# Performance work log

Hardware: AMD Instinct MI355X
Metric: run time of the kernel (lower is better)

Reference implementation:

```python
import jax, jax.numpy as jnp
import numpy as np

P1 = np.uint32(2654435761)
P2 = np.uint32(805459861)

LEVELS = 16
N_MIN = 16
GROWTH = 1.5
TABLE_SIZE = 524288
FEAT_DIM = 2


def _make_seeds_u32(levels):
    cA = np.uint64(15485907386658061715)
    cB = np.uint64(11400714819323198485)
    ls = np.arange(levels, dtype=np.uint64)
    u = (cA ^ (ls * cB))  # uint64 wraparound
    return (u & np.uint64(0xFFFFFFFF)).astype(np.uint32)


def setup_inputs() -> dict:
    key = jax.random.key(0)
    k1, k2, k3 = jax.random.split(key, 3)
    B = 8
    H = 256
    tile = 1024
    x0 = jax.random.uniform(k1, (B,), dtype=jnp.float32) * (tile - H)
    y0 = jax.random.uniform(k2, (B,), dtype=jnp.float32) * (tile - H)
    tables = jax.random.uniform(k3, (TABLE_SIZE, FEAT_DIM), dtype=jnp.float32,
                                minval=-0.01, maxval=0.01)
    seeds = jnp.asarray(_make_seeds_u32(LEVELS))
    level_N = jnp.asarray(
        [int(round(N_MIN * GROWTH ** l)) for l in range(LEVELS)], dtype=jnp.float32)
    return {"x0": x0, "y0": y0, "tables": tables, "seeds": seeds,
            "level_N": level_N, "memorized_crop_size": H,
            "complete_tile_size": tile}


def _hash2d(ix, iy, seed_u, T):
    # Instant-NGP style spatial hash, uint32 wraparound, per-level seed.
    h = (ix.astype(jnp.uint32) * P1) ^ (iy.astype(jnp.uint32) * P2) ^ seed_u
    return (h % jnp.uint32(T)).astype(jnp.int32)


def reference(x0, y0, tables, seeds, level_N, memorized_crop_size, complete_tile_size):
    B = x0.shape[0]
    H = W = int(memorized_crop_size)
    L = seeds.shape[0]
    T, F = tables.shape
    N = H * W

    xs = jnp.arange(H, dtype=jnp.float32)
    yy, xx = jnp.meshgrid(xs, xs, indexing='ij')          # [H, W]
    pxf = (xx[None] + x0[:, None, None]).reshape(B, N)     # [B, N]
    pyf = (yy[None] + y0[:, None, None]).reshape(B, N)

    scales = level_N / jnp.float32(complete_tile_size)     # [L]
    xyn_x = pxf[:, None, :] * scales[None, :, None]        # [B, L, N]
    xyn_y = pyf[:, None, :] * scales[None, :, None]

    ix0 = jnp.floor(xyn_x).astype(jnp.int32)
    iy0 = jnp.floor(xyn_y).astype(jnp.int32)
    ix1 = ix0 + 1
    iy1 = iy0 + 1
    fx = (xyn_x - ix0)[..., None]                          # [B, L, N, 1]
    fy = (xyn_y - iy0)[..., None]

    s = seeds[None, :, None]                               # [1, L, 1] uint32
    f00 = tables[_hash2d(ix0, iy0, s, T)]                  # [B, L, N, F]
    f10 = tables[_hash2d(ix1, iy0, s, T)]
    f01 = tables[_hash2d(ix0, iy1, s, T)]
    f11 = tables[_hash2d(ix1, iy1, s, T)]

    enc = ((1.0 - fx) * (1.0 - fy) * f00 + fx * (1.0 - fy) * f10
           + (1.0 - fx) * fy * f01 + fx * fy * f11)        # [B, L, N, F]

    enc = jnp.transpose(enc, (0, 2, 1, 3)).reshape(B, H, W, L * F)
    return jnp.transpose(enc, (0, 3, 1, 2))                # [B, L*F, H, W]
```

## Files before the change

kernel.cpp:

```cpp
#include <hip/hip_runtime.h>
#include <stdint.h>

#define HASH_T 524288u
#define HASH_MASK (HASH_T - 1u)
#define PRIME1 2654435761u
#define PRIME2 805459861u


#define HASHES(l, h00, h10, h01, h11, FX, FY)                          \
    float FX, FY; uint32_t h00, h10, h01, h11;                         \
    {                                                                  \
        const float s_ = level_N[l] * inv_tile;                        \
        const float xn_ = px * s_, yn_ = py * s_;                      \
        const int ix_ = (int)xn_, iy_ = (int)yn_;     \
        FX = xn_ - (float)ix_; FY = yn_ - (float)iy_;                  \
        const uint32_t hx0_ = (uint32_t)ix_ * PRIME1, hx1_ = hx0_ + PRIME1; \
        const uint32_t hy0_ = (uint32_t)iy_ * PRIME2, hy1_ = hy0_ + PRIME2; \
        const uint32_t sd_ = seeds[l];                                 \
        h00 = (hx0_ ^ hy0_ ^ sd_) & HASH_MASK;                         \
        h10 = (hx1_ ^ hy0_ ^ sd_) & HASH_MASK;                         \
        h01 = (hx0_ ^ hy1_ ^ sd_) & HASH_MASK;                         \
        h11 = (hx1_ ^ hy1_ ^ sd_) & HASH_MASK;                         \
    }

#define LOADS(h00, h10, h01, h11, f00, f10, f01, f11)                  \
    const float2 f00 = tab2[h00], f10 = tab2[h10],                     \
                 f01 = tab2[h01], f11 = tab2[h11];

#define STOREL(l, FX, FY, f00, f10, f01, f11)                          \
    {                                                                  \
        const float gx_ = 1.0f - FX, gy_ = 1.0f - FY;                  \
        const float w00_ = gx_ * gy_, w10_ = FX * gy_;                 \
        const float w01_ = gx_ * FY,  w11_ = FX * FY;                  \
        const float e0_ = w00_ * f00.x + w10_ * f10.x + w01_ * f01.x + w11_ * f11.x; \
        const float e1_ = w00_ * f00.y + w10_ * f10.y + w01_ * f01.y + w11_ * f11.y; \
        __builtin_nontemporal_store(e0_, outp + (size_t)(2 * (l)) * 65536u);     \
        __builtin_nontemporal_store(e1_, outp + (size_t)(2 * (l) + 1) * 65536u); \
    }

#define PAIR(la, lb)                                                   \
    {                                                                  \
        HASHES(la, a00, a10, a01, a11, fxa, fya)                       \
        HASHES(lb, b00, b10, b01, b11, fxb, fyb)                       \
        LOADS(a00, a10, a01, a11, fa00, fa10, fa01, fa11)              \
        LOADS(b00, b10, b01, b11, fb00, fb10, fb01, fb11)              \
        STOREL(la, fxa, fya, fa00, fa10, fa01, fa11)                   \
        STOREL(lb, fxb, fyb, fb00, fb10, fb01, fb11)                   \
    }

#define SINGLE(l)                                                      \
    {                                                                  \
        HASHES(l, c00, c10, c01, c11, fxc, fyc)                        \
        LOADS(c00, c10, c01, c11, fc00, fc10, fc01, fc11)              \
        STOREL(l, fxc, fyc, fc00, fc10, fc01, fc11)                    \
    }

__global__ __launch_bounds__(256) void lia_hashgrid_kernel(
    const float* __restrict__ x0,
    const float* __restrict__ y0,
    const float* __restrict__ tables,
    const uint32_t* __restrict__ seeds,
    const float* __restrict__ level_N,
    const int* __restrict__ tile_p,
    float* __restrict__ out)
{
    const int gid = blockIdx.x * 256 + threadIdx.x;
    const int j = gid & 255;
    const int i = (gid >> 8) & 255;
    const int bt = gid >> 16;
    const int b = bt / 3;
    const int third = bt - 3 * b;

    const float inv_tile = 1.0f / (float)(*tile_p);
    const float px = (float)j + x0[b];
    const float py = (float)i + y0[b];

    const float2* __restrict__ tab2 = (const float2*)tables;
    float* outp = out + (size_t)b * 32u * 65536u + (size_t)(i * 256 + j);

    if (third == 0) {
        PAIR(0, 3)
        PAIR(6, 9)
        PAIR(12, 15)
    } else if (third == 1) {
        PAIR(1, 4)
        PAIR(7, 10)
        SINGLE(13)
    } else {
        PAIR(2, 5)
        PAIR(8, 11)
        SINGLE(14)
    }
}

extern "C" void kernel_launch(void* const* d_in, const int* in_sizes, int n_in,
                              void* d_out, int out_size, void* d_ws, size_t ws_size,
                              hipStream_t stream) {
    const float*    x0      = (const float*)d_in[0];
    const float*    y0      = (const float*)d_in[1];
    const float*    tables  = (const float*)d_in[2];
    const uint32_t* seeds   = (const uint32_t*)d_in[3];
    const float*    level_N = (const float*)d_in[4];
    const int*      tile_p  = (const int*)d_in[6];
    float*          out     = (float*)d_out;

    const int B = in_sizes[0];
    const int n_blocks = B * 3 * 256;

    lia_hashgrid_kernel<<<n_blocks, 256, 0, stream>>>(
        x0, y0, tables, seeds, level_N, tile_p, out);
}
```

Measured before the change: 69.60 us.

## Stage coarse-level hash table entries in LDS per row block

Each block now covers one image row for one batch/level-group. For the four coarsest levels of its group it hashes the two grid rows it needs, gathers those table entries into LDS once, and then interpolates from LDS. The finer levels still use direct global gathers. Block indexing is also reordered so consecutive blocks share a row across batch/third. This is meant to cut redundant global gathers at coarse levels, at the cost of a __syncthreads, LDS traffic and extra index arithmetic. It assumes the coarse-level footprint fits in 1024 entries.

```diff
diff --git a/kernel.cpp b/kernel.cpp
--- a/kernel.cpp
+++ b/kernel.cpp
@@ -1,8 +1,7 @@
 #include <hip/hip_runtime.h>
 #include <stdint.h>
 
-#define HASH_T 524288u
-#define HASH_MASK (HASH_T - 1u)
+#define HASH_MASK 524287u
 #define PRIME1 2654435761u
 #define PRIME2 805459861u
 
@@ -64,31 +63,83 @@
     const int* __restrict__ tile_p,
     float* __restrict__ out)
 {
-    const int gid = blockIdx.x * 256 + threadIdx.x;
-    const int j = gid & 255;
-    const int i = (gid >> 8) & 255;
-    const int bt = gid >> 16;
-    const int b = bt / 3;
-    const int third = bt - 3 * b;
+    __shared__ float2 lds[1024];
+
+    const int nbt = gridDim.x >> 8;
+    const int bid = blockIdx.x;
+    const int bt  = bid % nbt;
+    const int i   = bid / nbt;
+    const int b   = bt / 3;
+    const int third = bt % 3;
+    const int j   = threadIdx.x;
 
     const float inv_tile = 1.0f / (float)(*tile_p);
-    const float px = (float)j + x0[b];
+    const float xb = x0[b];
     const float py = (float)i + y0[b];
+    const float px = (float)j + xb;
 
     const float2* __restrict__ tab2 = (const float2*)tables;
     float* outp = out + (size_t)b * 32u * 65536u + (size_t)(i * 256 + j);
 
+    static const int LVT[3][4] = {{0,3,6,9},{1,4,7,10},{2,5,8,11}};
+    int lv[4]; float sc[4]; uint32_t sd[4];
+    int X0[4], IY[4], NX[4], OFF[4];
+    int off = 0;
+    #pragma unroll
+    for (int k = 0; k < 4; ++k) {
+        const int l = LVT[third][k];
+        lv[k] = l;
+        const float s = level_N[l] * inv_tile;
+        sc[k] = s;
+        sd[k] = seeds[l];
+        X0[k] = (int)(xb * s);
+        IY[k] = (int)(py * s);
+        NX[k] = (int)((xb + 255.0f) * s) - X0[k] + 2;
+        OFF[k] = off;
+        off += 2 * NX[k];
+    }
+
+    #pragma unroll
+    for (int k = 0; k < 4; ++k) {
+        const int nx = NX[k], tot = 2 * nx;
+        for (int idx = j; idx < tot; idx += 256) {
+            const int row = (idx >= nx) ? 1 : 0;
+            const int col = idx - row * nx;
+            const uint32_t ix = (uint32_t)(X0[k] + col);
+            const uint32_t iy = (uint32_t)(IY[k] + row);
+            const uint32_t h = (ix * PRIME1 ^ iy * PRIME2 ^ sd[k]) & HASH_MASK;
+            lds[OFF[k] + idx] = tab2[h];
+        }
+    }
+    __syncthreads();
+
+    #pragma unroll
+    for (int k = 0; k < 4; ++k) {
+        const float s = sc[k];
+        const float xn = px * s;
+        const int ixl = (int)xn;
+        const float fx = xn - (float)ixl;
+        const float yn = py * s;
+        const float fy = yn - (float)IY[k];
+        const int c = OFF[k] + (ixl - X0[k]);
+        const float2 f00 = lds[c];
+        const float2 f10 = lds[c + 1];
+        const float2 f01 = lds[c + NX[k]];
+        const float2 f11 = lds[c + NX[k] + 1];
+        const float gx = 1.0f - fx, gy = 1.0f - fy;
+        const float w00 = gx * gy, w10 = fx * gy;
+        const float w01 = gx * fy, w11 = fx * fy;
+        const float e0 = w00 * f00.x + w10 * f10.x + w01 * f01.x + w11 * f11.x;
+        const float e1 = w00 * f00.y + w10 * f10.y + w01 * f01.y + w11 * f11.y;
+        __builtin_nontemporal_store(e0, outp + (size_t)(2 * lv[k]) * 65536u);
+        __builtin_nontemporal_store(e1, outp + (size_t)(2 * lv[k] + 1) * 65536u);
+    }
+
     if (third == 0) {
-        PAIR(0, 3)
-        PAIR(6, 9)
         PAIR(12, 15)
     } else if (third == 1) {
-        PAIR(1, 4)
-        PAIR(7, 10)
         SINGLE(13)
     } else {
-        PAIR(2, 5)
-        PAIR(8, 11)
         SINGLE(14)
     }
 }
@@ -105,7 +156,7 @@
     float*          out     = (float*)d_out;
 
     const int B = in_sizes[0];
-    const int n_blocks = B * 3 * 256;
+    const int n_blocks = 256 * 3 * B;
 
     lia_hashgrid_kernel<<<n_blocks, 256, 0, stream>>>(
         x0, y0, tables, seeds, level_N, tile_p, out);
```

New measurement: 65.41 us. -6.0%, faster.

## Stage coarse-level hash cells in LDS per 4-row tile, gather fine levels directly

Applied to the files above, without the earlier changes.

Each block now covers a 4-row by 256-column strip of one batch image with 1024 threads. For levels 0–11 the block first gathers every table entry its strip touches into shared memory, so corner cells shared by neighbouring pixels are fetched once. Pixels then interpolate from LDS, while levels 12–15 keep the old direct global gathers. The aim is fewer redundant random global reads on coarse levels. The cost is a barrier, far fewer and larger blocks (lower occupancy and less latency hiding), and reliance on the LDS cell-range bounds matching the per-pixel floor computations.

```diff
diff --git a/kernel.cpp b/kernel.cpp
--- a/kernel.cpp
+++ b/kernel.cpp
@@ -1,8 +1,7 @@
 #include <hip/hip_runtime.h>
 #include <stdint.h>
 
-#define HASH_T 524288u
-#define HASH_MASK (HASH_T - 1u)
+#define HASH_MASK 524287u
 #define PRIME1 2654435761u
 #define PRIME2 805459861u
 
@@ -48,14 +47,7 @@
         STOREL(lb, fxb, fyb, fb00, fb10, fb01, fb11)                   \
     }
 
-#define SINGLE(l)                                                      \
-    {                                                                  \
-        HASHES(l, c00, c10, c01, c11, fxc, fyc)                        \
-        LOADS(c00, c10, c01, c11, fc00, fc10, fc01, fc11)              \
-        STOREL(l, fxc, fyc, fc00, fc10, fc01, fc11)                    \
-    }
-
-__global__ __launch_bounds__(256) void lia_hashgrid_kernel(
+__global__ __launch_bounds__(1024, 8) void lia_hashgrid_kernel(
     const float* __restrict__ x0,
     const float* __restrict__ y0,
     const float* __restrict__ tables,
@@ -64,33 +56,84 @@
     const int* __restrict__ tile_p,
     float* __restrict__ out)
 {
-    const int gid = blockIdx.x * 256 + threadIdx.x;
-    const int j = gid & 255;
-    const int i = (gid >> 8) & 255;
-    const int bt = gid >> 16;
-    const int b = bt / 3;
-    const int third = bt - 3 * b;
+    __shared__ float2 lds[6400];
+
+    const int bid = blockIdx.x;
+    const int b   = bid >> 6;
+    const int i0  = (bid & 63) << 2;
+    const int tid = threadIdx.x;
+    const int j   = tid & 255;
+    const int r   = tid >> 8;
+    const int i   = i0 + r;
 
     const float inv_tile = 1.0f / (float)(*tile_p);
-    const float px = (float)j + x0[b];
+    const float xb  = x0[b];
+    const float py0 = (float)i0 + y0[b];
+    const float px = (float)j + xb;
     const float py = (float)i + y0[b];
 
     const float2* __restrict__ tab2 = (const float2*)tables;
     float* outp = out + (size_t)b * 32u * 65536u + (size_t)(i * 256 + j);
 
-    if (third == 0) {
-        PAIR(0, 3)
-        PAIR(6, 9)
-        PAIR(12, 15)
-    } else if (third == 1) {
-        PAIR(1, 4)
-        PAIR(7, 10)
-        SINGLE(13)
-    } else {
-        PAIR(2, 5)
-        PAIR(8, 11)
-        SINGLE(14)
+    {
+        int off = 0;
+        #pragma unroll
+        for (int l = 0; l < 12; ++l) {
+            const float s = level_N[l] * inv_tile;
+            const uint32_t sd = seeds[l];
+            const int X0 = (int)(xb * s);
+            const int NX = (int)((xb + 255.0f) * s) - X0 + 2;
+            const int Y0 = (int)(py0 * s);
+            const int NY = (int)((py0 + 3.0f) * s) - Y0 + 2;
+            const int cells = NY * NX;
+            for (int idx = tid; idx < cells; idx += 1024) {
+                const int row = idx / NX;
+                const int col = idx - row * NX;
+                const uint32_t h = ((uint32_t)(X0 + col) * PRIME1
+                                  ^ (uint32_t)(Y0 + row) * PRIME2 ^ sd) & HASH_MASK;
+                lds[off + idx] = tab2[h];
+            }
+            off += cells;
+        }
     }
+    __syncthreads();
+
+    {
+        int off = 0;
+        #pragma unroll
+        for (int l = 0; l < 12; ++l) {
+            const float s = level_N[l] * inv_tile;
+            const int X0 = (int)(xb * s);
+            const int NX = (int)((xb + 255.0f) * s) - X0 + 2;
+            const int Y0 = (int)(py0 * s);
+            const int NY = (int)((py0 + 3.0f) * s) - Y0 + 2;
+
+            const float xn = px * s;
+            const int ix = (int)xn;
+            const float fx = xn - (float)ix;
+            const float yn = py * s;
+            const int iy = (int)yn;
+            const float fy = yn - (float)iy;
+
+            const int c = off + (iy - Y0) * NX + (ix - X0);
+            const float2 f00 = lds[c];
+            const float2 f10 = lds[c + 1];
+            const float2 f01 = lds[c + NX];
+            const float2 f11 = lds[c + NX + 1];
+
+            const float gx = 1.0f - fx, gy = 1.0f - fy;
+            const float w00 = gx * gy, w10 = fx * gy;
+            const float w01 = gx * fy, w11 = fx * fy;
+            const float e0 = w00 * f00.x + w10 * f10.x + w01 * f01.x + w11 * f11.x;
+            const float e1 = w00 * f00.y + w10 * f10.y + w01 * f01.y + w11 * f11.y;
+            __builtin_nontemporal_store(e0, outp + (size_t)(2 * l) * 65536u);
+            __builtin_nontemporal_store(e1, outp + (size_t)(2 * l + 1) * 65536u);
+            off += NY * NX;
+        }
+    }
+
+    PAIR(12, 13)
+    PAIR(14, 15)
 }
 
 extern "C" void kernel_launch(void* const* d_in, const int* in_sizes, int n_in,
@@ -105,8 +148,8 @@
     float*          out     = (float*)d_out;
 
     const int B = in_sizes[0];
-    const int n_blocks = B * 3 * 256;
+    const int n_blocks = B * 64;
 
-    lia_hashgrid_kernel<<<n_blocks, 256, 0, stream>>>(
+    lia_hashgrid_kernel<<<n_blocks, 1024, 0, stream>>>(
         x0, y0, tables, seeds, level_N, tile_p, out);
 }
```

Result: faster. 58.34 us (median of 2 runs) (-16.2%).
